# Performance work log

Hardware: AMD Instinct MI355X
Metric: run time of the kernel (lower is better)

The kernel has to match this reference:

```python
import jax, jax.numpy as jnp
import numpy as np
import math

DIM = 1280
NUM_HEADS = 16
HEAD_DIM = DIM // NUM_HEADS  # 80
SEQ = 3072


def setup_inputs() -> dict:
    key = jax.random.key(0)
    ks = jax.random.split(key, 6)
    hidden_states = jax.random.normal(ks[0], (SEQ, DIM), dtype=jnp.float32)
    cu_seqlens = jnp.array([0, 768, 1536, 2304, 3072], dtype=jnp.int32)
    # rotary angles for half the head dim, as produced by the vision rotary embedding
    rotary_pos_emb = jax.random.uniform(ks[1], (SEQ, HEAD_DIM // 2), dtype=jnp.float32) * 10.0
    qkv_w = jax.random.normal(ks[2], (3 * DIM, DIM), dtype=jnp.float32) * (1.0 / math.sqrt(DIM))
    qkv_b = jax.random.normal(ks[3], (3 * DIM,), dtype=jnp.float32) * 0.02
    proj_w = jax.random.normal(ks[4], (DIM, DIM), dtype=jnp.float32) * (1.0 / math.sqrt(DIM))
    proj_b = jax.random.normal(ks[5], (DIM,), dtype=jnp.float32) * 0.02
    return {"hidden_states": hidden_states, "cu_seqlens": cu_seqlens,
            "rotary_pos_emb": rotary_pos_emb, "qkv_w": qkv_w, "qkv_b": qkv_b,
            "proj_w": proj_w, "proj_b": proj_b}


def _rotate_half(x):
    half = x.shape[-1] // 2
    return jnp.concatenate([-x[..., half:], x[..., :half]], axis=-1)


def _apply_rotary(t, rotary_pos_emb):
    # t: [seq, heads, head_dim]; rotary_pos_emb: [seq, head_dim//2]
    emb = jnp.concatenate([rotary_pos_emb, rotary_pos_emb], axis=-1)  # [seq, head_dim]
    cos = jnp.cos(emb)[:, None, :]
    sin = jnp.sin(emb)[:, None, :]
    return t * cos + _rotate_half(t) * sin


def reference(hidden_states, cu_seqlens, rotary_pos_emb, qkv_w, qkv_b, proj_w, proj_b):
    seq = hidden_states.shape[0]
    qkv = hidden_states @ qkv_w.T + qkv_b                       # [seq, 3*dim]
    qkv = qkv.reshape(seq, 3, NUM_HEADS, HEAD_DIM)
    q, k, v = qkv[:, 0], qkv[:, 1], qkv[:, 2]                   # [seq, h, d]
    q = _apply_rotary(q, rotary_pos_emb)
    k = _apply_rotary(k, rotary_pos_emb)

    # block-diagonal mask: token i attends to token j iff same segment
    seg = jnp.searchsorted(cu_seqlens[1:], jnp.arange(seq), side='right')
    same = seg[:, None] == seg[None, :]                         # [seq, seq] bool
    neg = jnp.finfo(q.dtype).min
    add_mask = jnp.where(same, jnp.float32(0), neg).astype(q.dtype)

    scale = 1.0 / math.sqrt(HEAD_DIM)
    scores = jnp.einsum('nhd,mhd->hnm', q, k) * scale           # [h, seq, seq]
    scores = scores + add_mask[None, :, :]
    attn = jax.nn.softmax(scores.astype(jnp.float32), axis=-1).astype(q.dtype)
    out = jnp.einsum('hnm,mhd->nhd', attn, v).reshape(seq, DIM)
    return out @ proj_w.T + proj_b
```

## Files before the change

### kernel.cpp

```cpp
#include <hip/hip_runtime.h>

#define SEQ 3072
#define NH 16
#define HD 80
#define SEGLEN 768

typedef unsigned short u16;
typedef unsigned int u32;
typedef float f32x4 __attribute__((ext_vector_type(4)));
typedef __bf16 bf16x8 __attribute__((ext_vector_type(8)));
typedef short short8 __attribute__((ext_vector_type(8)));
typedef u16 u16x4 __attribute__((ext_vector_type(4)));

#define WAITV(N) asm volatile("s_waitcnt vmcnt(" #N ")" ::: "memory")

__device__ __forceinline__ u16 f2bf(float f) {
  u32 u = __builtin_bit_cast(u32, f);
  u32 r = u + 0x7fffu + ((u >> 16) & 1u);
  return (u16)(r >> 16);
}
__device__ __forceinline__ float bf2f(u16 x) {
  u32 u = ((u32)x) << 16;
  return __builtin_bit_cast(float, u);
}
__device__ __forceinline__ u16 f2bf_hw(float f) {
  __bf16 b = (__bf16)f;
  return __builtin_bit_cast(u16, b);
}

__device__ __forceinline__ f32x4 mfma16(short8 a, short8 b, f32x4 c) {
  return __builtin_amdgcn_mfma_f32_16x16x32_bf16(
      __builtin_bit_cast(bf16x8, a), __builtin_bit_cast(bf16x8, b), c, 0, 0, 0);
}

__device__ __forceinline__ void gload_lds16(const u16* g, u16* l) {
  __builtin_amdgcn_global_load_lds(
      (const __attribute__((address_space(1))) u32*)(g),
      (__attribute__((address_space(3))) u32*)(l), 16, 0, 0);
}

__global__ __launch_bounds__(256) void cvt3p(
    const float* __restrict__ a, u16* __restrict__ ao, int na,
    const float* __restrict__ b, u16* __restrict__ bo, int nb,
    const float* __restrict__ c, u16* __restrict__ co, int nc,
    u16* __restrict__ vt) {
  int i = blockIdx.x * 256 + threadIdx.x;
  if (i < na) {
    f32x4 v = ((const f32x4*)a)[i];
    u16x4 o = {f2bf(v[0]), f2bf(v[1]), f2bf(v[2]), f2bf(v[3])};
    ((u16x4*)ao)[i] = o;
  } else if (i < na + nb) {
    int n = i - na;
    int row = n / 320, col4 = n % 320;
    int dstrow = row;
    if (row < 2560) {
      int sec = row / 1280, rr = row - sec * 1280;
      int h = rr / 80, dd = rr % 80;
      dstrow = sec * 1280 + h * 80 + 2 * (dd % 40) + (dd >= 40 ? 1 : 0);
    }
    f32x4 v = ((const f32x4*)b)[n];
    u16x4 o = {f2bf(v[0]), f2bf(v[1]), f2bf(v[2]), f2bf(v[3])};
    ((u16x4*)bo)[dstrow * 320 + col4] = o;
  } else if (i < na + nb + nc) {
    int n = i - na - nb;
    f32x4 v = ((const f32x4*)c)[n];
    u16x4 o = {f2bf(v[0]), f2bf(v[1]), f2bf(v[2]), f2bf(v[3])};
    ((u16x4*)co)[n] = o;
  } else if (i < na + nb + nc + 12288) {
    int j = i - na - nb - nc;
    int h = j / 768, s4 = (j % 768) * 4;
    u16x4 o = {0x3F80, 0x3F80, 0x3F80, 0x3F80};
    *(u16x4*)(vt + (size_t)(h * 96 + 80) * 3072 + s4) = o;
  }
}

__global__ __launch_bounds__(512) void gemm_192(
    const u16* __restrict__ A, const u16* __restrict__ B,
    const float* __restrict__ bias, const float* __restrict__ rpe,
    u16* __restrict__ qbg, u16* __restrict__ kbg, u16* __restrict__ vtg,
    int K) {
  __shared__ u16 LB[2 * 28672];
  char* lds = (char*)LB;
  const int tid = threadIdx.x, lane = tid & 63, w = tid >> 6;
  const int wm = w >> 2, wn = w & 3;
  const int lr = lane & 15, lg = lane >> 4;
  const int br = blockIdx.y * 192, bc = blockIdx.x * 256;
  const int NT = K >> 6;

  f32x4 acc[6][4];
#pragma unroll
  for (int m = 0; m < 6; ++m)
#pragma unroll
    for (int n = 0; n < 4; ++n) acc[m][n] = (f32x4){0.f, 0.f, 0.f, 0.f};

  const int chA0 = w * 96 + lane, chA1 = w * 96 + 64 + lane;
  const int chB0 = w * 128 + lane, chB1 = w * 128 + 64 + lane;
  auto srcptr = [&](const u16* Mx, int base, int ch) {
    int row = ch >> 2, sl = ch & 3;
    return Mx + (size_t)(base + row) * K + (((sl - (row >> 1)) & 3) << 3);
  };
  const u16* sA0 = srcptr(A, br, chA0);
  const u16* sA1 = srcptr(A, br, chA1 < 768 ? chA1 : chA0);
  const u16* sB0 = srcptr(B, bc, chB0);
  const u16* sB1 = srcptr(B, bc, chB1);

  auto stgA = [&](int kcol, int buf, int half) {
    char* hb = lds + buf * 57344 + half * 12288;
    gload_lds16(sA0 + kcol, (u16*)(hb + chA0 * 16));
    if (lane < 32) gload_lds16(sA1 + kcol, (u16*)(hb + chA1 * 16));
  };
  auto stgB = [&](int kcol, int buf, int half) {
    char* hb = lds + buf * 57344 + 24576 + half * 16384;
    gload_lds16(sB0 + kcol, (u16*)(hb + chB0 * 16));
    gload_lds16(sB1 + kcol, (u16*)(hb + chB1 * 16));
  };

  int aoff[6], boff[4];
#pragma unroll
  for (int m = 0; m < 6; ++m) {
    int row = wm * 96 + m * 16 + lr;
    aoff[m] = row * 64 + ((lg + (row >> 1)) & 3) * 16;
  }
#pragma unroll
  for (int n = 0; n < 4; ++n) {
    int row = wn * 64 + n * 16 + lr;
    boff[n] = row * 64 + ((lg + (row >> 1)) & 3) * 16;
  }

  stgA(0, 0, 0); stgB(0, 0, 0);
  stgA(32, 0, 1); stgB(32, 0, 1);
  WAITV(4);
  __builtin_amdgcn_s_barrier();

  for (int t = 0; t < NT; ++t) {
    const int p = t & 1;
    const char* bufb = lds + p * 57344;
#pragma unroll
    for (int q = 0; q < 2; ++q) {
      const char* Ah = bufb + q * 12288;
      const char* Bh = bufb + 24576 + q * 16384;
      short8 af[6], bf[4];
#pragma unroll
      for (int m = 0; m < 6; ++m) af[m] = *(const short8*)(Ah + aoff[m]);
#pragma unroll
      for (int n = 0; n < 4; ++n) bf[n] = *(const short8*)(Bh + boff[n]);
      if (t + 1 < NT) {
        stgA((t + 1) * 64 + q * 32, p ^ 1, q);
        stgB((t + 1) * 64 + q * 32, p ^ 1, q);
      }
      __builtin_amdgcn_s_setprio(1);
#pragma unroll
      for (int m = 0; m < 6; ++m)
#pragma unroll
        for (int n = 0; n < 4; ++n) acc[m][n] = mfma16(af[m], bf[n], acc[m][n]);
      __builtin_amdgcn_s_setprio(0);
      if (t + 1 < NT) {
        WAITV(4);
        __builtin_amdgcn_s_barrier();
      } else if (q == 0) {
        WAITV(0);
        __builtin_amdgcn_s_barrier();
      }
    }
  }

  const int sec = blockIdx.x / 5;
  __syncthreads();
  {
    float bv[4];
#pragma unroll
    for (int n = 0; n < 4; ++n) {
      int col_l = wn * 64 + n * 16 + lr;
      int gc = (bc - sec * 1280) + col_l;
      int h = gc / 80, cc = gc % 80;
      int d = (sec < 2) ? ((cc >> 1) + ((cc & 1) ? 40 : 0)) : cc;
      bv[n] = bias[sec * 1280 + h * 80 + d];
    }
#pragma unroll
    for (int n = 0; n < 4; ++n) {
      int col_l = wn * 64 + n * 16 + lr;
#pragma unroll
      for (int m = 0; m < 6; ++m) {
        int rowb = wm * 96 + m * 16 + lg * 4;
#pragma unroll
        for (int r = 0; r < 4; ++r)
          *(u16*)(lds + (size_t)(rowb + r) * 514 + col_l * 2) = f2bf(acc[m][n][r] + bv[n]);
      }
    }
  }
  __syncthreads();
  if (sec == 2) {
#pragma unroll
    for (int e = 0; e < 96; ++e) {
      int idx = e * 512 + tid;
      int col = idx / 192, row = idx % 192;
      u16 val = *(const u16*)(lds + (size_t)row * 514 + col * 2);
      int gc = bc - 2560 + col;
      int h = gc / 80, d = gc % 80;
      vtg[(size_t)(h * 96 + d) * 3072 + br + row] = val;
    }
  } else {
    u16* outb = sec ? kbg : qbg;
    const float scale = sec ? 1.0f : 0.16129841769519493f;
#pragma unroll
    for (int e = 0; e < 48; ++e) {
      int idx = e * 512 + tid;
      int row = idx >> 7, cp = idx & 127;
      float v0 = bf2f(*(const u16*)(lds + (size_t)row * 514 + cp * 4));
      float v1 = bf2f(*(const u16*)(lds + (size_t)row * 514 + cp * 4 + 2));
      int gc = bc - sec * 1280 + cp * 2;
      int h = gc / 80, dpair = (gc % 80) >> 1;
      float ang = rpe[(br + row) * 40 + dpair];
      float s, c;
      sincosf(ang, &s, &c);
      size_t ob_ = (size_t)(br + row) * 1280 + h * 80 + dpair;
      outb[ob_] = f2bf((v0 * c - v1 * s) * scale);
      outb[ob_ + 40] = f2bf((v1 * c + v0 * s) * scale);
    }
  }
}

template <int OUT_BF16, int WM, int WN>
__global__ __launch_bounds__(256) void gemm_p3(
    const u16* __restrict__ A, const u16* __restrict__ B,
    const float* __restrict__ bias, void* __restrict__ Cv,
    int M, int N, int K) {
  constexpr int BM = 32 * WM, BN = 32 * WN;
  constexpr int ROWS = BM + BN;
  constexpr int L = ROWS / 64;
  static_assert(L == 3, "tuned for L=3");
  __shared__ u16 LB[3][ROWS * 32];
  const int tid = threadIdx.x, lane = tid & 63, w = tid >> 6;
  const int wr = (w >> 1) * (WM * 16), wc = (w & 1) * (WN * 16);
  const int lr = lane & 15, lg = lane >> 4;
  const int gy = gridDim.y;
  const int fc = blockIdx.x * gy + blockIdx.y;
  const int cpx = (gridDim.x * gy) >> 3;
  const int f = (fc & 7) * cpx + (fc >> 3);
  const int bx = f / gy, by = f % gy;
  const int br = by * BM, bc = bx * BN;
  const int NT = K >> 5;

  f32x4 acc[WM][WN];
#pragma unroll
  for (int m = 0; m < WM; ++m)
#pragma unroll
    for (int n = 0; n < WN; ++n) acc[m][n] = (f32x4){0.f, 0.f, 0.f, 0.f};

  const u16* sp[L];
#pragma unroll
  for (int c = 0; c < L; ++c) {
    int ch = c * 256 + tid;
    int row = ch >> 2, sl = ch & 3;
    int scol = ((sl - (row >> 1)) & 3) << 3;
    sp[c] = (row < BM ? A + (br + row) * (size_t)K
                      : B + (bc + row - BM) * (size_t)K) + scol;
  }
  auto stage = [&](int t, int buf) {
#pragma unroll
    for (int c = 0; c < L; ++c)
      gload_lds16(sp[c] + t * 32, &LB[buf][(c * 256 + tid) * 8]);
  };

  int aoff[WM], boff[WN];
#pragma unroll
  for (int m = 0; m < WM; ++m) {
    int row = wr + m * 16 + lr;
    aoff[m] = row * 64 + ((lg + (row >> 1)) & 3) * 16;
  }
#pragma unroll
  for (int n = 0; n < WN; ++n) {
    int row = BM + wc + n * 16 + lr;
    boff[n] = row * 64 + ((lg + (row >> 1)) & 3) * 16;
  }

  auto step = [&](int t, int buf, bool issue, int wn) {
    if (issue) stage(t + 2, (t + 2) % 3);
    const char* base = (const char*)&LB[buf][0];
    short8 af[WM], bf[WN];
#pragma unroll
    for (int m = 0; m < WM; ++m) af[m] = *(const short8*)(base + aoff[m]);
#pragma unroll
    for (int n = 0; n < WN; ++n) bf[n] = *(const short8*)(base + boff[n]);
#pragma unroll
    for (int m = 0; m < WM; ++m)
#pragma unroll
      for (int n = 0; n < WN; ++n) acc[m][n] = mfma16(af[m], bf[n], acc[m][n]);
    if (wn == 3) WAITV(3);
    else if (wn == 0) WAITV(0);
    if (wn >= 0) __builtin_amdgcn_s_barrier();
  };

  stage(0, 0);
  stage(1, 1);
  WAITV(3);
  __builtin_amdgcn_s_barrier();

  int t = 0;
  for (; t + 3 <= NT - 2; t += 3) {
    step(t + 0, 0, true, 3);
    step(t + 1, 1, true, 3);
    step(t + 2, 2, true, 3);
  }
  step(NT - 4, 0, true, 3);
  step(NT - 3, 1, true, 3);
  step(NT - 2, 2, false, 0);
  step(NT - 1, 0, false, -1);

#pragma unroll
  for (int n = 0; n < WN; ++n) {
    int col = bc + wc + n * 16 + lr;
    float bv = bias[col];
#pragma unroll
    for (int m = 0; m < WM; ++m) {
      int rowb = br + wr + m * 16 + lg * 4;
#pragma unroll
      for (int r = 0; r < 4; ++r) {
        float v = acc[m][n][r] + bv;
        if (OUT_BF16)
          ((u16*)Cv)[(rowb + r) * N + col] = f2bf(v);
        else
          ((float*)Cv)[(rowb + r) * N + col] = v;
      }
    }
  }
}

__global__ __launch_bounds__(256) void attn_kern(
    const u16* __restrict__ qb, const u16* __restrict__ kb,
    const u16* __restrict__ vt, u16* __restrict__ ob) {
  __shared__ u16 SH[26176];
  char* shb = (char*)SH;
  const int tid = threadIdx.x, lane = tid & 63, w = tid >> 6;
  const int lr = lane & 15, lg = lane >> 4;
  const int xcd = blockIdx.x & 7, t = blockIdx.x >> 3;
  const int qt = t % 12, shhi = t / 12;
  const int sh = xcd + shhi * 8;
  const int seg = sh >> 4, h = sh & 15;
  const int qrow = seg * SEGLEN + qt * 64 + w * 16 + lr;

  short8 qf[3];
#pragma unroll
  for (int kk = 0; kk < 3; ++kk) {
    int d = kk * 32 + lg * 8;
    if (d < 80)
      qf[kk] = *(const short8*)(qb + qrow * 1280 + h * 80 + d);
    else
      qf[kk] = (short8){0, 0, 0, 0, 0, 0, 0, 0};
  }
  f32x4 oa[6];
#pragma unroll
  for (int n = 0; n < 6; ++n) oa[n] = (f32x4){0.f, 0.f, 0.f, 0.f};

  const u16* kseg = kb + seg * SEGLEN * 1280 + h * 80;
  const u16* vseg = vt + (h * 96) * 3072 + seg * SEGLEN;

  auto stageK = [&](int buf, int it) {
    const u16* kbase = kseg + it * 64 * 1280;
#pragma unroll
    for (int c = 0; c < 4; ++c) {
      int ch = c * 256 + tid;
      int kv = ch >> 4, sl = ch & 15;
      gload_lds16(kbase + kv * 1280 + ((sl ^ (kv & 7)) << 3),
                  (u16*)(shb + buf * 16384 + ch * 16));
    }
  };
  auto stageV = [&](int it) {
    const u16* vbase = vseg + it * 64;
#pragma unroll
    for (int c = 0; c < 3; ++c) {
      int ch = c * 256 + tid;
      if (ch < 648) {
        int d = ch >> 3, sl = ch & 7;
        gload_lds16(vbase + d * 3072 + ((sl ^ (d & 7)) << 3),
                    (u16*)(shb + 32768 + ch * 16));
      }
    }
  };

  stageK(0, 0);
  stageV(0);
  __syncthreads();
  int cur = 0;
  char* PsW = shb + 43136 + w * 2304;
  const char* Vc = shb + 32768;

  for (int it = 0; it < 12; ++it) {
    if (it > 0) stageV(it);
    if (it < 11) stageK(cur ^ 1, it + 1);
    const char* Kc = shb + cur * 16384;
    f32x4 sf[4];
#pragma unroll
    for (int n = 0; n < 4; ++n) {
      sf[n] = (f32x4){0.f, 0.f, 0.f, 0.f};
#pragma unroll
      for (int kk = 0; kk < 3; ++kk) {
        int row = n * 16 + lr;
        int X = kk * 64 + lg * 16;
        short8 kf = *(const short8*)(Kc + row * 256 + (X ^ ((row & 7) << 4)));
        __builtin_amdgcn_s_setprio(1);
        sf[n] = mfma16(qf[kk], kf, sf[n]);
        __builtin_amdgcn_s_setprio(0);
      }
    }
#pragma unroll
    for (int r = 0; r < 4; ++r) {
      float p0 = exp2f(sf[0][r] - 20.0f), p1 = exp2f(sf[1][r] - 20.0f);
      float p2 = exp2f(sf[2][r] - 20.0f), p3 = exp2f(sf[3][r] - 20.0f);
      int offb = (lg * 4 + r) * 144 + lr * 2;
      *(u16*)(PsW + offb + ((lg ^ 0) << 5)) = f2bf_hw(p0);
      *(u16*)(PsW + offb + ((lg ^ 1) << 5)) = f2bf_hw(p1);
      *(u16*)(PsW + offb + ((lg ^ 2) << 5)) = f2bf_hw(p2);
      *(u16*)(PsW + offb + ((lg ^ 3) << 5)) = f2bf_hw(p3);
    }
    __syncthreads();
#pragma unroll
    for (int kt = 0; kt < 2; ++kt) {
      short8 pf = *(const short8*)(PsW + lr * 144 +
                                   ((((kt << 1) + (lg >> 1)) ^ (lr >> 2)) << 5) +
                                   ((lg & 1) << 4));
#pragma unroll
      for (int n = 0; n < 6; ++n) {
        int dcol = n * 16 + lr;
        int X = kt * 64 + lg * 16;
        short8 vf = *(const short8*)(Vc + dcol * 128 + (X ^ ((dcol & 7) << 4)));
        __builtin_amdgcn_s_setprio(1);
        oa[n] = mfma16(pf, vf, oa[n]);
        __builtin_amdgcn_s_setprio(0);
      }
    }
    __syncthreads();
    cur ^= 1;
  }
#pragma unroll
  for (int r = 0; r < 4; ++r) {
    float lsum = __shfl(oa[5][r], lane & 48, 64);
    float linv = 1.0f / lsum;
    int orow = seg * SEGLEN + qt * 64 + w * 16 + lg * 4 + r;
#pragma unroll
    for (int n = 0; n < 5; ++n)
      ob[orow * 1280 + h * 80 + n * 16 + lr] = f2bf(oa[n][r] * linv);
  }
}

extern "C" void kernel_launch(void* const* d_in, const int* in_sizes, int n_in,
                              void* d_out, int out_size, void* d_ws, size_t ws_size,
                              hipStream_t stream) {
  const float* hs = (const float*)d_in[0];
  const float* rpe = (const float*)d_in[2];
  const float* qkvw = (const float*)d_in[3];
  const float* qkv_b = (const float*)d_in[4];
  const float* pw = (const float*)d_in[5];
  const float* pb = (const float*)d_in[6];
  float* out = (float*)d_out;

  char* ws = (char*)d_ws;
  u16* hsb = (u16*)(ws);
  u16* wqkvb = (u16*)(ws + 7864320);
  u16* wprojb = (u16*)(ws + 17694720);
  u16* qb = (u16*)(ws + 20971520);
  u16* kb = (u16*)(ws + 28835840);
  u16* vt = (u16*)(ws + 36700160);
  u16* aob = (u16*)(ws + 46137344);

  cvt3p<<<10288, 256, 0, stream>>>(hs, hsb, 983040, qkvw, wqkvb, 1228800,
                                   pw, wprojb, 409600, vt);
  gemm_192<<<dim3(15, 16), 512, 0, stream>>>(hsb, wqkvb, qkv_b, rpe, qb, kb, vt, 1280);
  attn_kern<<<768, 256, 0, stream>>>(qb, kb, vt, aob);
  gemm_p3<0, 2, 4><<<dim3(10, 48), 256, 0, stream>>>(aob, wprojb, pb, out, 3072, 1280, 1280);
}
```

Measured before the change: 112.9 us.

## Retile QKV GEMM to 192x128 with 256 threads and triple-buffered K32 pipeline

Replaces the 192x256, 512-thread QKV GEMM with a 192x128 tile run by 256 threads. A unified A/B staging scheme uses three LDS buffers and 32-wide K steps, prefetching two stages ahead, and the main loop is unrolled by three. The grid doubles to 480 blocks, which should fill the CUs better and keep more loads in flight. In exchange each block reuses less data, so total global traffic for the shared operand rises, and the s_setprio hints around the MFMA block are dropped.

```diff
diff --git a/kernel.cpp b/kernel.cpp
--- a/kernel.cpp
+++ b/kernel.cpp
@@ -74,18 +74,18 @@
   }
 }
 
-__global__ __launch_bounds__(512) void gemm_192(
+__global__ __launch_bounds__(256) void gemm_qkv(
     const u16* __restrict__ A, const u16* __restrict__ B,
     const float* __restrict__ bias, const float* __restrict__ rpe,
     u16* __restrict__ qbg, u16* __restrict__ kbg, u16* __restrict__ vtg,
     int K) {
-  __shared__ u16 LB[2 * 28672];
-  char* lds = (char*)LB;
+  constexpr int BM = 192, BN = 128, ROWS = 320;
+  __shared__ u16 LB[3][ROWS * 32];
   const int tid = threadIdx.x, lane = tid & 63, w = tid >> 6;
-  const int wm = w >> 2, wn = w & 3;
+  const int wr = (w >> 1) * 96, wc = (w & 1) * 64;
   const int lr = lane & 15, lg = lane >> 4;
-  const int br = blockIdx.y * 192, bc = blockIdx.x * 256;
-  const int NT = K >> 6;
+  const int br = blockIdx.y * BM, bc = blockIdx.x * BN;
+  const int NT = K >> 5;
 
   f32x4 acc[6][4];
 #pragma unroll
@@ -93,84 +93,74 @@
 #pragma unroll
     for (int n = 0; n < 4; ++n) acc[m][n] = (f32x4){0.f, 0.f, 0.f, 0.f};
 
-  const int chA0 = w * 96 + lane, chA1 = w * 96 + 64 + lane;
-  const int chB0 = w * 128 + lane, chB1 = w * 128 + 64 + lane;
-  auto srcptr = [&](const u16* Mx, int base, int ch) {
+  const u16* sp[5];
+#pragma unroll
+  for (int c = 0; c < 5; ++c) {
+    int ch = c * 256 + tid;
     int row = ch >> 2, sl = ch & 3;
-    return Mx + (size_t)(base + row) * K + (((sl - (row >> 1)) & 3) << 3);
-  };
-  const u16* sA0 = srcptr(A, br, chA0);
-  const u16* sA1 = srcptr(A, br, chA1 < 768 ? chA1 : chA0);
-  const u16* sB0 = srcptr(B, bc, chB0);
-  const u16* sB1 = srcptr(B, bc, chB1);
-
-  auto stgA = [&](int kcol, int buf, int half) {
-    char* hb = lds + buf * 57344 + half * 12288;
-    gload_lds16(sA0 + kcol, (u16*)(hb + chA0 * 16));
-    if (lane < 32) gload_lds16(sA1 + kcol, (u16*)(hb + chA1 * 16));
-  };
-  auto stgB = [&](int kcol, int buf, int half) {
-    char* hb = lds + buf * 57344 + 24576 + half * 16384;
-    gload_lds16(sB0 + kcol, (u16*)(hb + chB0 * 16));
-    gload_lds16(sB1 + kcol, (u16*)(hb + chB1 * 16));
+    int scol = ((sl - (row >> 1)) & 3) << 3;
+    sp[c] = (row < BM ? A + (size_t)(br + row) * K
+                      : B + (size_t)(bc + row - BM) * K) + scol;
+  }
+  auto stage = [&](int t, int buf) {
+#pragma unroll
+    for (int c = 0; c < 5; ++c)
+      gload_lds16(sp[c] + t * 32, &LB[buf][(c * 256 + tid) * 8]);
   };
 
   int aoff[6], boff[4];
 #pragma unroll
   for (int m = 0; m < 6; ++m) {
-    int row = wm * 96 + m * 16 + lr;
+    int row = wr + m * 16 + lr;
     aoff[m] = row * 64 + ((lg + (row >> 1)) & 3) * 16;
   }
 #pragma unroll
   for (int n = 0; n < 4; ++n) {
-    int row = wn * 64 + n * 16 + lr;
+    int row = BM + wc + n * 16 + lr;
     boff[n] = row * 64 + ((lg + (row >> 1)) & 3) * 16;
   }
 
-  stgA(0, 0, 0); stgB(0, 0, 0);
-  stgA(32, 0, 1); stgB(32, 0, 1);
-  WAITV(4);
+  auto step = [&](int t, int buf, bool issue, int wn) {
+    if (issue) stage(t + 2, (t + 2) % 3);
+    const char* base = (const char*)&LB[buf][0];
+    short8 af[6], bf[4];
+#pragma unroll
+    for (int m = 0; m < 6; ++m) af[m] = *(const short8*)(base + aoff[m]);
+#pragma unroll
+    for (int n = 0; n < 4; ++n) bf[n] = *(const short8*)(base + boff[n]);
+#pragma unroll
+    for (int m = 0; m < 6; ++m)
+#pragma unroll
+      for (int n = 0; n < 4; ++n) acc[m][n] = mfma16(af[m], bf[n], acc[m][n]);
+    if (wn == 5) WAITV(5);
+    else if (wn == 0) WAITV(0);
+    if (wn >= 0) __builtin_amdgcn_s_barrier();
+  };
+
+  stage(0, 0);
+  stage(1, 1);
+  WAITV(5);
   __builtin_amdgcn_s_barrier();
 
-  for (int t = 0; t < NT; ++t) {
-    const int p = t & 1;
-    const char* bufb = lds + p * 57344;
-#pragma unroll
-    for (int q = 0; q < 2; ++q) {
-      const char* Ah = bufb + q * 12288;
-      const char* Bh = bufb + 24576 + q * 16384;
-      short8 af[6], bf[4];
-#pragma unroll
-      for (int m = 0; m < 6; ++m) af[m] = *(const short8*)(Ah + aoff[m]);
-#pragma unroll
-      for (int n = 0; n < 4; ++n) bf[n] = *(const short8*)(Bh + boff[n]);
-      if (t + 1 < NT) {
-        stgA((t + 1) * 64 + q * 32, p ^ 1, q);
-        stgB((t + 1) * 64 + q * 32, p ^ 1, q);
-      }
-      __builtin_amdgcn_s_setprio(1);
-#pragma unroll
-      for (int m = 0; m < 6; ++m)
-#pragma unroll
-        for (int n = 0; n < 4; ++n) acc[m][n] = mfma16(af[m], bf[n], acc[m][n]);
-      __builtin_amdgcn_s_setprio(0);
-      if (t + 1 < NT) {
-        WAITV(4);
-        __builtin_amdgcn_s_barrier();
-      } else if (q == 0) {
-        WAITV(0);
-        __builtin_amdgcn_s_barrier();
-      }
-    }
-  }
-
-  const int sec = blockIdx.x / 5;
+  int t = 0;
+  for (; t + 3 <= NT - 2; t += 3) {
+    step(t + 0, 0, true, 5);
+    step(t + 1, 1, true, 5);
+    step(t + 2, 2, true, 5);
+  }
+  step(NT - 4, 0, true, 5);
+  step(NT - 3, 1, true, 5);
+  step(NT - 2, 2, false, 0);
+  step(NT - 1, 0, false, -1);
+
+  const int sec = blockIdx.x / 10;
+  char* lds = (char*)&LB[0][0];
   __syncthreads();
   {
     float bv[4];
 #pragma unroll
     for (int n = 0; n < 4; ++n) {
-      int col_l = wn * 64 + n * 16 + lr;
+      int col_l = wc + n * 16 + lr;
       int gc = (bc - sec * 1280) + col_l;
       int h = gc / 80, cc = gc % 80;
       int d = (sec < 2) ? ((cc >> 1) + ((cc & 1) ? 40 : 0)) : cc;
@@ -178,13 +168,13 @@
     }
 #pragma unroll
     for (int n = 0; n < 4; ++n) {
-      int col_l = wn * 64 + n * 16 + lr;
+      int col_l = wc + n * 16 + lr;
 #pragma unroll
       for (int m = 0; m < 6; ++m) {
-        int rowb = wm * 96 + m * 16 + lg * 4;
+        int rowb = wr + m * 16 + lg * 4;
 #pragma unroll
         for (int r = 0; r < 4; ++r)
-          *(u16*)(lds + (size_t)(rowb + r) * 514 + col_l * 2) = f2bf(acc[m][n][r] + bv[n]);
+          *(u16*)(lds + (size_t)(rowb + r) * 258 + col_l * 2) = f2bf(acc[m][n][r] + bv[n]);
       }
     }
   }
@@ -192,9 +182,9 @@
   if (sec == 2) {
 #pragma unroll
     for (int e = 0; e < 96; ++e) {
-      int idx = e * 512 + tid;
+      int idx = e * 256 + tid;
       int col = idx / 192, row = idx % 192;
-      u16 val = *(const u16*)(lds + (size_t)row * 514 + col * 2);
+      u16 val = *(const u16*)(lds + (size_t)row * 258 + col * 2);
       int gc = bc - 2560 + col;
       int h = gc / 80, d = gc % 80;
       vtg[(size_t)(h * 96 + d) * 3072 + br + row] = val;
@@ -204,10 +194,10 @@
     const float scale = sec ? 1.0f : 0.16129841769519493f;
 #pragma unroll
     for (int e = 0; e < 48; ++e) {
-      int idx = e * 512 + tid;
-      int row = idx >> 7, cp = idx & 127;
-      float v0 = bf2f(*(const u16*)(lds + (size_t)row * 514 + cp * 4));
-      float v1 = bf2f(*(const u16*)(lds + (size_t)row * 514 + cp * 4 + 2));
+      int idx = e * 256 + tid;
+      int row = idx >> 6, cp = idx & 63;
+      float v0 = bf2f(*(const u16*)(lds + (size_t)row * 258 + cp * 4));
+      float v1 = bf2f(*(const u16*)(lds + (size_t)row * 258 + cp * 4 + 2));
       int gc = bc - sec * 1280 + cp * 2;
       int h = gc / 80, dpair = (gc % 80) >> 1;
       float ang = rpe[(br + row) * 40 + dpair];
@@ -465,7 +455,7 @@
 
   cvt3p<<<10288, 256, 0, stream>>>(hs, hsb, 983040, qkvw, wqkvb, 1228800,
                                    pw, wprojb, 409600, vt);
-  gemm_192<<<dim3(15, 16), 512, 0, stream>>>(hsb, wqkvb, qkv_b, rpe, qb, kb, vt, 1280);
+  gemm_qkv<<<dim3(30, 16), 256, 0, stream>>>(hsb, wqkvb, qkv_b, rpe, qb, kb, vt, 1280);
   attn_kern<<<768, 256, 0, stream>>>(qb, kb, vt, aob);
   gemm_p3<0, 2, 4><<<dim3(10, 48), 256, 0, stream>>>(aob, wprojb, pb, out, 3072, 1280, 1280);
 }
```

Result: slower. 142.0 us (+25.8%).
